# Kernel optimization log

Measured on AMD Instinct MI355X. Metric: run time of the kernel, lower is better.

## Reference

```python
import jax, jax.numpy as jnp
import numpy as np

D_MODEL = 1024
HEADS = 16
HEAD_DIM = D_MODEL // HEADS
SEQ_LEN = 2048
BATCH = 2
LN_EPS = 1e-5


def _layernorm(x, gamma, beta):
    mu = jnp.mean(x, axis=-1, keepdims=True)
    var = jnp.var(x, axis=-1, keepdims=True)
    return (x - mu) * jax.lax.rsqrt(var + LN_EPS) * gamma + beta


def setup_inputs() -> dict:
    key = jax.random.key(0)
    ks = jax.random.split(key, 12)
    d, h = D_MODEL, 4 * D_MODEL
    s = lambda fan_in: 1.0 / np.sqrt(fan_in)
    return {
        "x": jax.random.normal(ks[0], (BATCH, SEQ_LEN, d), dtype=jnp.float32),
        "W_qkv": jax.random.uniform(ks[1], (d, 3 * d), minval=-s(d), maxval=s(d)),
        "b_qkv": jax.random.uniform(ks[2], (3 * d,), minval=-s(d), maxval=s(d)),
        "W1": jax.random.uniform(ks[3], (d, h), minval=-s(d), maxval=s(d)),
        "b1": jax.random.uniform(ks[4], (h,), minval=-s(d), maxval=s(d)),
        "W2": jax.random.uniform(ks[5], (h, d), minval=-s(h), maxval=s(h)),
        "b2": jax.random.uniform(ks[6], (d,), minval=-s(h), maxval=s(h)),
        "ln1_g": jnp.ones((d,), jnp.float32),
        "ln1_b": jnp.zeros((d,), jnp.float32),
        "ln2_g": jnp.ones((d,), jnp.float32),
        "ln2_b": jnp.zeros((d,), jnp.float32),
    }


def reference(x, W_qkv, b_qkv, W1, b1, W2, b2, ln1_g, ln1_b, ln2_g, ln2_b):
    B, T, C = x.shape
    # QKV projection -> [B, T, 3, H, hs] -> q,k,v each [B, H, T, hs]
    qkv = (x @ W_qkv + b_qkv).reshape(B, T, 3, HEADS, HEAD_DIM)
    qkv = jnp.transpose(qkv, (2, 0, 3, 1, 4))
    q, k, v = qkv[0], qkv[1], qkv[2]
    # Naive causal attention with full [B,H,T,T] score matrix (matches source)
    A = jnp.einsum("bhqd,bhkd->bhqk", q, k) / jnp.sqrt(jnp.float32(HEAD_DIM))
    causal = jnp.tril(jnp.ones((T, T), dtype=bool))
    A = jnp.where(causal, A, -jnp.inf)
    A = jax.nn.softmax(A, axis=-1)
    attn = jnp.einsum("bhqk,bhkd->bhqd", A, v)  # [B,H,T,hs]
    attn = jnp.transpose(attn, (0, 2, 1, 3)).reshape(B, T, C)
    # Residual + LN, FFN, residual + LN (dropout=0 / eval)
    h = _layernorm(x + attn, ln1_g, ln1_b)
    ff = jax.nn.relu(h @ W1 + b1) @ W2 + b2
    return _layernorm(h + ff, ln2_g, ln2_b)
```

## Files before the change

### kernel.cpp

```cpp
#include <hip/hip_runtime.h>

#define D_MODEL 1024
#define HEADS   16
#define HEAD_DIM 64
#define SEQ     2048
#define BATCH   2
#define ROWS    (BATCH*SEQ)
#define FFDIM   4096

typedef __attribute__((ext_vector_type(8))) short short8;
typedef __attribute__((ext_vector_type(4))) float f32x4;
typedef __attribute__((ext_vector_type(4))) unsigned short us4;

typedef const __attribute__((address_space(1))) unsigned int* gptr_t;
typedef __attribute__((address_space(3))) unsigned int* lptr_t;

__device__ __forceinline__ unsigned short f2bf(float f){
  unsigned int x = __float_as_uint(f);
  x += 0x7fffu + ((x >> 16) & 1u);
  return (unsigned short)(x >> 16);
}

__device__ __forceinline__ float wave_sum(float x){
  #pragma unroll
  for (int off = 32; off; off >>= 1) x += __shfl_xor(x, off);
  return x;
}

__global__ __launch_bounds__(256) void cast_bf16_kernel(const float* __restrict__ in,
                                                        unsigned short* __restrict__ out, int n4){
  int i = blockIdx.x * 256 + threadIdx.x;
  if (i >= n4) return;
  float4 v = *(const float4*)(in + (size_t)i * 4);
  us4 o;
  o[0] = f2bf(v.x); o[1] = f2bf(v.y); o[2] = f2bf(v.z); o[3] = f2bf(v.w);
  *(us4*)(out + (size_t)i * 4) = o;
}

__global__ __launch_bounds__(256) void transpose_cast_kernel(const float* __restrict__ in,
                                                             unsigned short* __restrict__ out,
                                                             int R, int C){
  __shared__ float tile[32][33];
  const int bc = blockIdx.x * 32, br = blockIdx.y * 32;
  const int tx = threadIdx.x & 31, ty = threadIdx.x >> 5;
  #pragma unroll
  for (int j = 0; j < 4; ++j)
    tile[ty + 8*j][tx] = in[(size_t)(br + ty + 8*j) * C + bc + tx];
  __syncthreads();
  #pragma unroll
  for (int j = 0; j < 4; ++j)
    out[(size_t)(bc + ty + 8*j) * R + br + tx] = f2bf(tile[tx][ty + 8*j]);
}

template<int EPI>
__global__ __launch_bounds__(256) void gemm_kernel(const unsigned short* __restrict__ A,
                                                   const unsigned short* __restrict__ BT,
                                                   const float* __restrict__ bias,
                                                   int M, int N, int K, int kchunk,
                                                   int gx, int gy,
                                                   float* __restrict__ outF,
                                                   unsigned short* __restrict__ qo,
                                                   unsigned short* __restrict__ ko,
                                                   unsigned short* __restrict__ vT){
  __shared__ __align__(16) unsigned short Alds[2][128 * 32];
  __shared__ __align__(16) unsigned short Blds[2][128 * 32];
  const int tid = threadIdx.x;
  const int lane = tid & 63;
  const int wid = tid >> 6;
  const int wr = wid >> 1, wc = wid & 1;
  const int lrow = lane & 15, lgrp = lane >> 4;

  const int nwg = gridDim.x;
  const int cpx = nwg >> 3;
  const int wg = (blockIdx.x & 7) * cpx + (blockIdx.x >> 3);
  const int nx = wg % gx;
  const int rest = wg / gx;
  const int my = rest % gy;
  const int sk = rest / gy;

  const int m0 = my * 128, n0 = nx * 128;
  const int kbase0 = sk * kchunk;
  const int sr = lane >> 2, sc = (lane & 3) * 8;

  f32x4 acc[4][4];
  #pragma unroll
  for (int i = 0; i < 4; ++i)
    #pragma unroll
    for (int j = 0; j < 4; ++j)
      acc[i][j] = f32x4{0.f, 0.f, 0.f, 0.f};

  #pragma unroll
  for (int it = 0; it < 2; ++it){
    const int c = wid * 2 + it;
    const int r = c * 16 + sr;
    __builtin_amdgcn_global_load_lds(
        (gptr_t)(const void*)(A + (size_t)(m0 + r) * K + kbase0 + sc),
        (lptr_t)(void*)(&Alds[0][c * 512]), 16, 0, 0);
    __builtin_amdgcn_global_load_lds(
        (gptr_t)(const void*)(BT + (size_t)(n0 + r) * K + kbase0 + sc),
        (lptr_t)(void*)(&Blds[0][c * 512]), 16, 0, 0);
  }

  const int nk = kchunk >> 5;
  int cur = 0;
  for (int kt = 0; kt < nk; ++kt){
    __syncthreads();
    if (kt + 1 < nk){
      const int kb = kbase0 + (kt + 1) * 32;
      #pragma unroll
      for (int it = 0; it < 2; ++it){
        const int c = wid * 2 + it;
        const int r = c * 16 + sr;
        __builtin_amdgcn_global_load_lds(
            (gptr_t)(const void*)(A + (size_t)(m0 + r) * K + kb + sc),
            (lptr_t)(void*)(&Alds[cur ^ 1][c * 512]), 16, 0, 0);
        __builtin_amdgcn_global_load_lds(
            (gptr_t)(const void*)(BT + (size_t)(n0 + r) * K + kb + sc),
            (lptr_t)(void*)(&Blds[cur ^ 1][c * 512]), 16, 0, 0);
      }
    }
    short8 af[4], bfr[4];
    #pragma unroll
    for (int f = 0; f < 4; ++f){
      af[f]  = *(const short8*)&Alds[cur][(wr * 64 + f * 16 + lrow) * 32 + lgrp * 8];
      bfr[f] = *(const short8*)&Blds[cur][(wc * 64 + f * 16 + lrow) * 32 + lgrp * 8];
    }
    __builtin_amdgcn_s_setprio(1);
    #pragma unroll
    for (int i = 0; i < 4; ++i)
      #pragma unroll
      for (int j = 0; j < 4; ++j)
        acc[i][j] = __builtin_amdgcn_mfma_f32_16x16x32_bf16(af[i], bfr[j], acc[i][j], 0, 0, 0);
    __builtin_amdgcn_s_setprio(0);
    cur ^= 1;
  }

  #pragma unroll
  for (int i = 0; i < 4; ++i){
    const int rg = m0 + wr * 64 + i * 16 + lgrp * 4;
    #pragma unroll
    for (int j = 0; j < 4; ++j){
      const int cg = n0 + wc * 64 + j * 16 + lrow;
      if constexpr (EPI == 0){
        const float bb = bias[cg];
        const int which = cg >> 10, rem = cg & 1023;
        const int hh = rem >> 6, dd = rem & 63;
        const int bb_ = rg >> 11, tt = rg & 2047;
        const size_t bh = (size_t)(bb_ * HEADS + hh);
        if (which == 2){
          us4 pk;
          #pragma unroll
          for (int r = 0; r < 4; ++r) pk[r] = f2bf(acc[i][j][r] + bb);
          *(us4*)(vT + (bh * 64 + dd) * SEQ + tt) = pk;
        } else {
          unsigned short* dst = which ? ko : qo;
          const float sc2 = which ? 1.0f : 0.18033688f;
          #pragma unroll
          for (int r = 0; r < 4; ++r)
            dst[(bh * SEQ + tt + r) * 64 + dd] = f2bf((acc[i][j][r] + bb) * sc2);
        }
      } else {
        float* outP = outF + (size_t)sk * M * N;
        #pragma unroll
        for (int r = 0; r < 4; ++r)
          outP[(size_t)(rg + r) * N + cg] = acc[i][j][r];
      }
    }
  }
}

template<int EPI>
__global__ __launch_bounds__(512, 1) void gemm8p_kernel(const unsigned short* __restrict__ A,
                                                        const unsigned short* __restrict__ BT,
                                                        const float* __restrict__ bias,
                                                        int M, int N, int K, int kchunk,
                                                        int gx, int gy,
                                                        unsigned short* __restrict__ outH){
  __shared__ __align__(16) unsigned short Ab[2][2][256 * 32];
  __shared__ __align__(16) unsigned short Bb[2][2][256 * 32];
  const int tid = threadIdx.x, lane = tid & 63, wid = tid >> 6;
  const int wm = wid >> 2, wn = wid & 3;
  const int lr = lane & 15, g = lane >> 4;

  const int nwg = gridDim.x, cpx = nwg >> 3;
  const int wg = (blockIdx.x & 7) * cpx + (blockIdx.x >> 3);
  const int nx = wg % gx;
  const int rest = wg / gx;
  const int my = rest % gy;
  const int sk = rest / gy;
  const int m0 = my * 256, n0 = nx * 256, kb0 = sk * kchunk;
  const int nk = kchunk >> 6;

  f32x4 acc[8][4];
  #pragma unroll
  for (int i = 0; i < 8; ++i)
    #pragma unroll
    for (int j = 0; j < 4; ++j)
      acc[i][j] = f32x4{0.f, 0.f, 0.f, 0.f};

  auto STAGE = [&](int op, int t, int kh){
    const int d = t & 1;
    unsigned short* base = op ? &Bb[d][kh][0] : &Ab[d][kh][0];
    const unsigned short* src = op ? BT : A;
    const int r0 = op ? n0 : m0;
    #pragma unroll
    for (int j = 0; j < 2; ++j){
      const int L = tid + j * 512;
      const int row = L >> 2, c = L & 3;
      __builtin_amdgcn_global_load_lds(
          (gptr_t)(const void*)(src + (size_t)(r0 + row) * K + kb0 + t * 64 + kh * 32
                                + ((c ^ ((row >> 1) & 3)) << 3)),
          (lptr_t)(void*)(base + L * 8), 16, 0, 0);
    }
  };

  STAGE(0,0,0); STAGE(1,0,0); STAGE(0,0,1); STAGE(1,0,1);
  STAGE(0,1,0); STAGE(1,1,0); STAGE(0,1,1); STAGE(1,1,1);
  asm volatile("s_waitcnt vmcnt(12)" ::: "memory");
  __builtin_amdgcn_s_barrier();

  short8 afr[8], bfr[4];

  #define SYNC_NOV()                                              \
    __builtin_amdgcn_s_barrier();                                 \
    asm volatile("s_waitcnt lgkmcnt(0)" ::: "memory");            \
    __builtin_amdgcn_sched_barrier(0);

  for (int t = 0; t < nk; ++t){
    const int d = t & 1;
    #pragma unroll
    for (int i = 0; i < 8; ++i){
      const int row = wm * 128 + i * 16 + lr;
      afr[i] = *(const short8*)&Ab[d][0][row * 32 + ((g ^ ((row >> 1) & 3)) << 3)];
    }
    #pragma unroll
    for (int j = 0; j < 2; ++j){
      const int row = wn * 64 + j * 16 + lr;
      bfr[j] = *(const short8*)&Bb[d][0][row * 32 + ((g ^ ((row >> 1) & 3)) << 3)];
    }
    if (t >= 1 && t + 1 < nk) STAGE(1, t + 1, 1);
    SYNC_NOV()
    __builtin_amdgcn_s_setprio(1);
    #pragma unroll
    for (int i = 0; i < 8; ++i){
      acc[i][0] = __builtin_amdgcn_mfma_f32_16x16x32_bf16(afr[i], bfr[0], acc[i][0], 0, 0, 0);
      acc[i][1] = __builtin_amdgcn_mfma_f32_16x16x32_bf16(afr[i], bfr[1], acc[i][1], 0, 0, 0);
    }
    __builtin_amdgcn_s_setprio(0);
    __builtin_amdgcn_s_barrier();

    #pragma unroll
    for (int j = 0; j < 2; ++j){
      const int row = wn * 64 + (2 + j) * 16 + lr;
      bfr[2 + j] = *(const short8*)&Bb[d][0][row * 32 + ((g ^ ((row >> 1) & 3)) << 3)];
    }
    if (t + 2 < nk) STAGE(0, t + 2, 0);
    if (t + 2 < nk)      asm volatile("s_waitcnt vmcnt(10)" ::: "memory");
    else if (t + 1 < nk) asm volatile("s_waitcnt vmcnt(8)"  ::: "memory");
    else                 asm volatile("s_waitcnt vmcnt(0)"  ::: "memory");
    SYNC_NOV()
    __builtin_amdgcn_s_setprio(1);
    #pragma unroll
    for (int i = 0; i < 8; ++i){
      acc[i][2] = __builtin_amdgcn_mfma_f32_16x16x32_bf16(afr[i], bfr[2], acc[i][2], 0, 0, 0);
      acc[i][3] = __builtin_amdgcn_mfma_f32_16x16x32_bf16(afr[i], bfr[3], acc[i][3], 0, 0, 0);
    }
    __builtin_amdgcn_s_setprio(0);
    __builtin_amdgcn_s_barrier();

    #pragma unroll
    for (int i = 0; i < 8; ++i){
      const int row = wm * 128 + i * 16 + lr;
      afr[i] = *(const short8*)&Ab[d][1][row * 32 + ((g ^ ((row >> 1) & 3)) << 3)];
    }
    #pragma unroll
    for (int j = 0; j < 2; ++j){
      const int row = wn * 64 + j * 16 + lr;
      bfr[j] = *(const short8*)&Bb[d][1][row * 32 + ((g ^ ((row >> 1) & 3)) << 3)];
    }
    if (t + 2 < nk) STAGE(1, t + 2, 0);
    SYNC_NOV()
    __builtin_amdgcn_s_setprio(1);
    #pragma unroll
    for (int i = 0; i < 8; ++i){
      acc[i][0] = __builtin_amdgcn_mfma_f32_16x16x32_bf16(afr[i], bfr[0], acc[i][0], 0, 0, 0);
      acc[i][1] = __builtin_amdgcn_mfma_f32_16x16x32_bf16(afr[i], bfr[1], acc[i][1], 0, 0, 0);
    }
    __builtin_amdgcn_s_setprio(0);
    __builtin_amdgcn_s_barrier();

    #pragma unroll
    for (int j = 0; j < 2; ++j){
      const int row = wn * 64 + (2 + j) * 16 + lr;
      bfr[2 + j] = *(const short8*)&Bb[d][1][row * 32 + ((g ^ ((row >> 1) & 3)) << 3)];
    }
    if (t + 2 < nk) STAGE(0, t + 2, 1);
    if (t + 2 < nk)      asm volatile("s_waitcnt vmcnt(10)" ::: "memory");
    else if (t + 1 < nk) asm volatile("s_waitcnt vmcnt(4)"  ::: "memory");
    SYNC_NOV()
    __builtin_amdgcn_s_setprio(1);
    #pragma unroll
    for (int i = 0; i < 8; ++i){
      acc[i][2] = __builtin_amdgcn_mfma_f32_16x16x32_bf16(afr[i], bfr[2], acc[i][2], 0, 0, 0);
      acc[i][3] = __builtin_amdgcn_mfma_f32_16x16x32_bf16(afr[i], bfr[3], acc[i][3], 0, 0, 0);
    }
    __builtin_amdgcn_s_setprio(0);
    __builtin_amdgcn_s_barrier();
  }
  #undef SYNC_NOV

  #pragma unroll
  for (int i = 0; i < 8; ++i){
    const int rg = m0 + wm * 128 + i * 16 + g * 4;
    #pragma unroll
    for (int j = 0; j < 4; ++j){
      const int cg = n0 + wn * 64 + j * 16 + lr;
      if constexpr (EPI == 1){
        const float bb = bias[cg];
        #pragma unroll
        for (int r = 0; r < 4; ++r)
          outH[(size_t)(rg + r) * N + cg] = f2bf(fmaxf(acc[i][j][r] + bb, 0.f));
      } else {
        unsigned short* dst = outH + (size_t)sk * M * N;
        #pragma unroll
        for (int r = 0; r < 4; ++r)
          dst[(size_t)(rg + r) * N + cg] = f2bf(acc[i][j][r]);
      }
    }
  }
}

__global__ __launch_bounds__(256) void attn_mfma_kernel(const unsigned short* __restrict__ Qb,
                                                        const unsigned short* __restrict__ Kb,
                                                        const unsigned short* __restrict__ VT,
                                                        float* __restrict__ Op){
  __shared__ __align__(16) char Kl[2][8192];
  __shared__ __align__(16) char Vl[2][8192];
  __shared__ __align__(16) char Pl[4][4096];
  const int tid = threadIdx.x;
  const int w = tid >> 6, lane = tid & 63;
  const int lr = lane & 15, g = lane >> 4;

  const int bx = blockIdx.x, u = bx & 255, half = bx >> 8;
  const int g8 = u >> 5;
  const int qg = half ? g8 : 15 - g8;
  const int bh = u & 31;

  const int q0w = qg * 128 + w * 32;
  const int qA = q0w + lr, qB = qA + 16;

  const char* const KbB = (const char*)(Kb + (size_t)bh * SEQ * 64);
  const char* const VbB = (const char*)(VT + (size_t)bh * 64 * SEQ);
  char* const PbA = Pl[w];
  char* const PbB = Pl[w] + 2048;

  const unsigned short* qra = Qb + ((size_t)bh * SEQ + qA) * 64 + g * 8;
  const short8 qfA0 = *(const short8*)(qra);
  const short8 qfA1 = *(const short8*)(qra + 32);
  const short8 qfB0 = *(const short8*)(qra + 16 * 64);
  const short8 qfB1 = *(const short8*)(qra + 16 * 64 + 32);

  f32x4 oA[4], oB[4];
  #pragma unroll
  for (int dt = 0; dt < 4; ++dt){ oA[dt] = f32x4{0.f,0.f,0.f,0.f}; oB[dt] = f32x4{0.f,0.f,0.f,0.f}; }
  float lA = 0.f, lB = 0.f;
  const int swzl = (lr & 7) << 4;

  const int kbmax = 2 * qg + 1;

  short8 st[4];
  {
    #pragma unroll
    for (int c = 0; c < 2; ++c){
      const int L = c * 4096 + tid * 16;
      st[c] = *(const short8*)(KbB + L);
      const int row = L >> 7, col = L & 127;
      st[2 + c] = *(const short8*)(VbB + (size_t)row * 4096 + col);
    }
  }

  for (int kb = 0; kb <= kbmax; ++kb){
    const int p = kb & 1;
    const int k0 = kb * 64;

    #pragma unroll
    for (int c = 0; c < 2; ++c){
      const int L = c * 4096 + tid * 16;
      const int row = L >> 7, col = L & 127;
      const int dst = row * 128 + (col ^ ((row & 7) << 4));
      *(short8*)(Kl[p] + dst) = st[c];
      *(short8*)(Vl[p] + dst) = st[2 + c];
    }
    __syncthreads();

    if (kb < kbmax){
      #pragma unroll
      for (int c = 0; c < 2; ++c){
        const int L = c * 4096 + tid * 16;
        st[c] = *(const short8*)(KbB + (size_t)(kb + 1) * 8192 + L);
        const int row = L >> 7, col = L & 127;
        st[2 + c] = *(const short8*)(VbB + (size_t)row * 4096 + (size_t)(kb + 1) * 128 + col);
      }
    }

    f32x4 sA[4], sB[4];
    __builtin_amdgcn_s_setprio(1);
    #pragma unroll
    for (int kt = 0; kt < 4; ++kt){
      const int row = kt * 16 + lr;
      const int ro = row * 128, sw = (row & 7) << 4;
      const short8 kf0 = *(const short8*)(Kl[p] + ro + ((g * 16) ^ sw));
      const short8 kf1 = *(const short8*)(Kl[p] + ro + ((64 + g * 16) ^ sw));
      sA[kt] = __builtin_amdgcn_mfma_f32_16x16x32_bf16(kf0, qfA0, f32x4{0.f,0.f,0.f,0.f}, 0, 0, 0);
      sA[kt] = __builtin_amdgcn_mfma_f32_16x16x32_bf16(kf1, qfA1, sA[kt], 0, 0, 0);
      sB[kt] = __builtin_amdgcn_mfma_f32_16x16x32_bf16(kf0, qfB0, f32x4{0.f,0.f,0.f,0.f}, 0, 0, 0);
      sB[kt] = __builtin_amdgcn_mfma_f32_16x16x32_bf16(kf1, qfB1, sB[kt], 0, 0, 0);
    }
    __builtin_amdgcn_s_setprio(0);

    if (kb >= kbmax - 1){
      #pragma unroll
      for (int kt = 0; kt < 4; ++kt)
        #pragma unroll
        for (int r = 0; r < 4; ++r){
          const int key = k0 + kt * 16 + g * 4 + r;
          if (key > qA) sA[kt][r] = -INFINITY;
          if (key > qB) sB[kt][r] = -INFINITY;
        }
    }

    {
      float sum = 0.f;
      #pragma unroll
      for (int kt = 0; kt < 4; ++kt){
        #pragma unroll
        for (int r = 0; r < 4; ++r){
          const float pp = __builtin_amdgcn_exp2f(sA[kt][r]);
          sA[kt][r] = pp; sum += pp;
        }
        unsigned int p01, p23;
        asm("v_cvt_pk_bf16_f32 %0, %1, %2" : "=v"(p01) : "v"(sA[kt][0]), "v"(sA[kt][1]));
        asm("v_cvt_pk_bf16_f32 %0, %1, %2" : "=v"(p23) : "v"(sA[kt][2]), "v"(sA[kt][3]));
        uint2 pk; pk.x = p01; pk.y = p23;
        *(uint2*)(PbA + lr * 128 + ((kt * 32 + g * 8) ^ swzl)) = pk;
      }
      sum += __shfl_xor(sum, 16);
      sum += __shfl_xor(sum, 32);
      lA += sum;
    }
    {
      float sum = 0.f;
      #pragma unroll
      for (int kt = 0; kt < 4; ++kt){
        #pragma unroll
        for (int r = 0; r < 4; ++r){
          const float pp = __builtin_amdgcn_exp2f(sB[kt][r]);
          sB[kt][r] = pp; sum += pp;
        }
        unsigned int p01, p23;
        asm("v_cvt_pk_bf16_f32 %0, %1, %2" : "=v"(p01) : "v"(sB[kt][0]), "v"(sB[kt][1]));
        asm("v_cvt_pk_bf16_f32 %0, %1, %2" : "=v"(p23) : "v"(sB[kt][2]), "v"(sB[kt][3]));
        uint2 pk; pk.x = p01; pk.y = p23;
        *(uint2*)(PbB + lr * 128 + ((kt * 32 + g * 8) ^ swzl)) = pk;
      }
      sum += __shfl_xor(sum, 16);
      sum += __shfl_xor(sum, 32);
      lB += sum;
    }

    const short8 paA0 = *(const short8*)(PbA + lr * 128 + ((g * 16) ^ swzl));
    const short8 paA1 = *(const short8*)(PbA + lr * 128 + ((64 + g * 16) ^ swzl));
    const short8 paB0 = *(const short8*)(PbB + lr * 128 + ((g * 16) ^ swzl));
    const short8 paB1 = *(const short8*)(PbB + lr * 128 + ((64 + g * 16) ^ swzl));
    __builtin_amdgcn_s_setprio(1);
    #pragma unroll
    for (int dt = 0; dt < 4; ++dt){
      const int row = dt * 16 + lr;
      const int ro = row * 128, sw = (row & 7) << 4;
      const short8 vf0 = *(const short8*)(Vl[p] + ro + ((g * 16) ^ sw));
      const short8 vf1 = *(const short8*)(Vl[p] + ro + ((64 + g * 16) ^ sw));
      oA[dt] = __builtin_amdgcn_mfma_f32_16x16x32_bf16(paA0, vf0, oA[dt], 0, 0, 0);
      oA[dt] = __builtin_amdgcn_mfma_f32_16x16x32_bf16(paA1, vf1, oA[dt], 0, 0, 0);
      oB[dt] = __builtin_amdgcn_mfma_f32_16x16x32_bf16(paB0, vf0, oB[dt], 0, 0, 0);
      oB[dt] = __builtin_amdgcn_mfma_f32_16x16x32_bf16(paB1, vf1, oB[dt], 0, 0, 0);
    }
    __builtin_amdgcn_s_setprio(0);
  }

  const int b = bh >> 4, hh = bh & 15;
  {
    float lv[4];
    #pragma unroll
    for (int r = 0; r < 4; ++r) lv[r] = __shfl(lA, g * 4 + r);
    #pragma unroll
    for (int dt = 0; dt < 4; ++dt)
      #pragma unroll
      for (int r = 0; r < 4; ++r)
        Op[((size_t)(b * SEQ) + q0w + g * 4 + r) * D_MODEL + hh * 64 + dt * 16 + lr] = oA[dt][r] / lv[r];
  }
  {
    float lv[4];
    #pragma unroll
    for (int r = 0; r < 4; ++r) lv[r] = __shfl(lB, g * 4 + r);
    #pragma unroll
    for (int dt = 0; dt < 4; ++dt)
      #pragma unroll
      for (int r = 0; r < 4; ++r)
        Op[((size_t)(b * SEQ) + q0w + 16 + g * 4 + r) * D_MODEL + hh * 64 + dt * 16 + lr] = oB[dt][r] / lv[r];
  }
}

__global__ __launch_bounds__(256) void ln_kernel(const float* __restrict__ A,
                                                 const float* __restrict__ B1,
                                                 const unsigned short* __restrict__ P4,
                                                 size_t pstride,
                                                 const float* __restrict__ bias,
                                                 const float* __restrict__ g,
                                                 const float* __restrict__ be,
                                                 float* __restrict__ outF,
                                                 unsigned short* __restrict__ outH){
  const int row = blockIdx.x, tid = threadIdx.x;
  const size_t base = (size_t)row * D_MODEL + tid * 4;
  float4 va = *(const float4*)(A + base);
  float v0 = va.x, v1 = va.y, v2 = va.z, v3 = va.w;
  if (B1){
    float4 vb = *(const float4*)(B1 + base);
    v0 += vb.x; v1 += vb.y; v2 += vb.z; v3 += vb.w;
  }
  if (P4){
    #pragma unroll
    for (int p = 0; p < 4; ++p){
      us4 u = *(const us4*)(P4 + p * pstride + base);
      v0 += __uint_as_float((unsigned int)u[0] << 16);
      v1 += __uint_as_float((unsigned int)u[1] << 16);
      v2 += __uint_as_float((unsigned int)u[2] << 16);
      v3 += __uint_as_float((unsigned int)u[3] << 16);
    }
  }
  if (bias){
    float4 vd = *(const float4*)(bias + tid * 4);
    v0 += vd.x; v1 += vd.y; v2 += vd.z; v3 += vd.w;
  }
  float s  = v0 + v1 + v2 + v3;
  float ss = v0*v0 + v1*v1 + v2*v2 + v3*v3;
  s = wave_sum(s); ss = wave_sum(ss);
  __shared__ float red[8];
  const int w = tid >> 6, lane = tid & 63;
  if (!lane){ red[w] = s; red[4 + w] = ss; }
  __syncthreads();
  s  = red[0] + red[1] + red[2] + red[3];
  ss = red[4] + red[5] + red[6] + red[7];
  const float mu  = s * (1.0f / D_MODEL);
  const float var = ss * (1.0f / D_MODEL) - mu * mu;
  const float rstd = rsqrtf(var + 1e-5f);
  float4 gg = *(const float4*)(g  + tid * 4);
  float4 bb = *(const float4*)(be + tid * 4);
  const float r0 = (v0 - mu) * rstd * gg.x + bb.x;
  const float r1 = (v1 - mu) * rstd * gg.y + bb.y;
  const float r2 = (v2 - mu) * rstd * gg.z + bb.z;
  const float r3 = (v3 - mu) * rstd * gg.w + bb.w;
  float4 of; of.x = r0; of.y = r1; of.z = r2; of.w = r3;
  *(float4*)(outF + base) = of;
  if (outH){
    us4 oh; oh[0] = f2bf(r0); oh[1] = f2bf(r1); oh[2] = f2bf(r2); oh[3] = f2bf(r3);
    *(us4*)(outH + base) = oh;
  }
}

__global__ __launch_bounds__(256) void ln2f_kernel(const float* __restrict__ A,
                                                   const float* __restrict__ B1,
                                                   const float* __restrict__ bias,
                                                   const float* __restrict__ g,
                                                   const float* __restrict__ be,
                                                   float* __restrict__ outF){
  const int row = blockIdx.x, tid = threadIdx.x;
  const size_t base = (size_t)row * D_MODEL + tid * 4;
  float4 va = *(const float4*)(A + base);
  float4 vb = *(const float4*)(B1 + base);
  float4 vd = *(const float4*)(bias + tid * 4);
  float v0 = va.x + vb.x + vd.x, v1 = va.y + vb.y + vd.y;
  float v2 = va.z + vb.z + vd.z, v3 = va.w + vb.w + vd.w;
  float s  = v0 + v1 + v2 + v3;
  float ss = v0*v0 + v1*v1 + v2*v2 + v3*v3;
  s = wave_sum(s); ss = wave_sum(ss);
  __shared__ float red[8];
  const int w = tid >> 6, lane = tid & 63;
  if (!lane){ red[w] = s; red[4 + w] = ss; }
  __syncthreads();
  s  = red[0] + red[1] + red[2] + red[3];
  ss = red[4] + red[5] + red[6] + red[7];
  const float mu  = s * (1.0f / D_MODEL);
  const float var = ss * (1.0f / D_MODEL) - mu * mu;
  const float rstd = rsqrtf(var + 1e-5f);
  float4 gg = *(const float4*)(g  + tid * 4);
  float4 bb = *(const float4*)(be + tid * 4);
  float4 of;
  of.x = (v0 - mu) * rstd * gg.x + bb.x;
  of.y = (v1 - mu) * rstd * gg.y + bb.y;
  of.z = (v2 - mu) * rstd * gg.z + bb.z;
  of.w = (v3 - mu) * rstd * gg.w + bb.w;
  *(float4*)(outF + base) = of;
}

extern "C" void kernel_launch(void* const* d_in, const int* in_sizes, int n_in,
                              void* d_out, int out_size, void* d_ws, size_t ws_size,
                              hipStream_t stream){
  (void)in_sizes; (void)n_in; (void)out_size;
  const float* x     = (const float*)d_in[0];
  const float* W_qkv = (const float*)d_in[1];
  const float* b_qkv = (const float*)d_in[2];
  const float* W1    = (const float*)d_in[3];
  const float* b1    = (const float*)d_in[4];
  const float* W2    = (const float*)d_in[5];
  const float* b2    = (const float*)d_in[6];
  const float* ln1g  = (const float*)d_in[7];
  const float* ln1b  = (const float*)d_in[8];
  const float* ln2g  = (const float*)d_in[9];
  const float* ln2b  = (const float*)d_in[10];

  char* ws = (char*)d_ws;
  const size_t MB = 1024ull * 1024ull;
  unsigned short* WqkvT = (unsigned short*)(ws + 0 * MB);
  unsigned short* W1T   = (unsigned short*)(ws + 6 * MB);
  unsigned short* W2T   = (unsigned short*)(ws + 14 * MB);
  unsigned short* xbf   = (unsigned short*)(ws + 22 * MB);
  unsigned short* qB    = (unsigned short*)(ws + 30 * MB);
  unsigned short* kB    = (unsigned short*)(ws + 39 * MB);
  unsigned short* vT    = (unsigned short*)(ws + 48 * MB);
  float* attn = (float*)(ws + 57 * MB);
  float* hF           = (float*)(ws + 30 * MB);
  unsigned short* hB  = (unsigned short*)(ws + 46 * MB);
  unsigned short* ff1 = (unsigned short*)(ws + 54 * MB);
  unsigned short* pbf = (unsigned short*)(ws + 86 * MB);
  float* p0           = (float*)(ws + 86 * MB);

  const int use8p = (ws_size >= 118 * MB);

  cast_bf16_kernel<<<4096, 256, 0, stream>>>(x, xbf, ROWS * D_MODEL / 4);
  transpose_cast_kernel<<<dim3(96, 32), 256, 0, stream>>>(W_qkv, WqkvT, 1024, 3072);
  transpose_cast_kernel<<<dim3(128, 32), 256, 0, stream>>>(W1, W1T, 1024, 4096);
  transpose_cast_kernel<<<dim3(32, 128), 256, 0, stream>>>(W2, W2T, 4096, 1024);

  gemm_kernel<0><<<768, 256, 0, stream>>>(
      xbf, WqkvT, b_qkv, ROWS, 3072, 1024, 1024, 24, 32, nullptr, qB, kB, vT);

  attn_mfma_kernel<<<512, 256, 0, stream>>>(qB, kB, vT, attn);

  ln_kernel<<<ROWS, 256, 0, stream>>>(x, attn, nullptr, 0, nullptr, ln1g, ln1b, hF, hB);

  gemm8p_kernel<1><<<256, 512, 0, stream>>>(
      hB, W1T, b1, ROWS, FFDIM, 1024, 1024, 16, 16, ff1);

  if (use8p){
    gemm8p_kernel<4><<<256, 512, 0, stream>>>(
        ff1, W2T, nullptr, ROWS, 1024, FFDIM, 1024, 4, 16, pbf);
    ln_kernel<<<ROWS, 256, 0, stream>>>(hF, nullptr, pbf, (size_t)ROWS * 1024, b2,
                                        ln2g, ln2b, (float*)d_out, nullptr);
  } else {
    gemm_kernel<3><<<256, 256, 0, stream>>>(
        ff1, W2T, nullptr, ROWS, 1024, FFDIM, FFDIM, 8, 32, p0, nullptr, nullptr, nullptr);
    ln2f_kernel<<<ROWS, 256, 0, stream>>>(hF, p0, b2, ln2g, ln2b, (float*)d_out);
  }
}
```

Baseline: 200.5 us.

## Restructure FFN GEMM main loop into two-phase double-buffered register pipeline

Replaces the four-phase per-iteration schedule of the 256x256 FFN GEMM with a two-phase one. Each phase issues 32 MFMAs on one K-half while LDS reads for the next half go into a second register set. Global-to-LDS prefetch is now one tile ahead per half instead of two, which cuts barriers per K step from eight to two. The cost is extra VGPRs for the duplicated fragment registers and a shallower global prefetch depth, which may expose memory latency.

New measurement: 215.1 us. 7.2% more time.

```diff
diff --git a/kernel.cpp b/kernel.cpp
--- a/kernel.cpp
+++ b/kernel.cpp
@@ -170,7 +170,7 @@
 }
 
 template<int EPI>
-__global__ __launch_bounds__(512, 1) void gemm8p_kernel(const unsigned short* __restrict__ A,
+__global__ __launch_bounds__(512, 1) void gemm2h_kernel(const unsigned short* __restrict__ A,
                                                         const unsigned short* __restrict__ BT,
                                                         const float* __restrict__ bias,
                                                         int M, int N, int K, int kchunk,
@@ -199,8 +199,8 @@
       acc[i][j] = f32x4{0.f, 0.f, 0.f, 0.f};
 
   auto STAGE = [&](int op, int t, int kh){
-    const int d = t & 1;
-    unsigned short* base = op ? &Bb[d][kh][0] : &Ab[d][kh][0];
+    const int d_ = t & 1;
+    unsigned short* base = op ? &Bb[d_][kh][0] : &Ab[d_][kh][0];
     const unsigned short* src = op ? BT : A;
     const int r0 = op ? n0 : m0;
     #pragma unroll
@@ -214,100 +214,65 @@
     }
   };
 
+  short8 afA[8], bfA[4], afB[8], bfB[4];
+
+  #define READS(da, db, d_, kh_)                                                          \
+    _Pragma("unroll")                                                                     \
+    for (int i = 0; i < 8; ++i){                                                          \
+      const int row = wm * 128 + i * 16 + lr;                                             \
+      da[i] = *(const short8*)&Ab[d_][kh_][row * 32 + ((g ^ ((row >> 1) & 3)) << 3)];     \
+    }                                                                                     \
+    _Pragma("unroll")                                                                     \
+    for (int j = 0; j < 4; ++j){                                                          \
+      const int row = wn * 64 + j * 16 + lr;                                              \
+      db[j] = *(const short8*)&Bb[d_][kh_][row * 32 + ((g ^ ((row >> 1) & 3)) << 3)];     \
+    }
+
+  #define MFMA32(sa, sb)                                                                  \
+    _Pragma("unroll")                                                                     \
+    for (int i = 0; i < 8; ++i)                                                           \
+      _Pragma("unroll")                                                                   \
+      for (int j = 0; j < 4; ++j)                                                         \
+        acc[i][j] = __builtin_amdgcn_mfma_f32_16x16x32_bf16(sa[i], sb[j], acc[i][j], 0, 0, 0);
+
   STAGE(0,0,0); STAGE(1,0,0); STAGE(0,0,1); STAGE(1,0,1);
-  STAGE(0,1,0); STAGE(1,1,0); STAGE(0,1,1); STAGE(1,1,1);
-  asm volatile("s_waitcnt vmcnt(12)" ::: "memory");
+  if (nk > 1){ STAGE(0,1,0); STAGE(1,1,0); }
+  if (nk > 1) asm volatile("s_waitcnt vmcnt(8)" ::: "memory");
+  else        asm volatile("s_waitcnt vmcnt(4)" ::: "memory");
   __builtin_amdgcn_s_barrier();
-
-  short8 afr[8], bfr[4];
-
-  #define SYNC_NOV()                                              \
-    __builtin_amdgcn_s_barrier();                                 \
-    asm volatile("s_waitcnt lgkmcnt(0)" ::: "memory");            \
+  READS(afA, bfA, 0, 0)
+
+  for (int t = 0; t < nk; ++t){
+    const int d = t & 1, dn = d ^ 1;
+
+    if (t + 1 < nk) asm volatile("s_waitcnt vmcnt(4)" ::: "memory");
+    else            asm volatile("s_waitcnt vmcnt(0)" ::: "memory");
+    __builtin_amdgcn_s_barrier();
+    if (t + 1 < nk){ STAGE(0, t + 1, 1); STAGE(1, t + 1, 1); }
+    READS(afB, bfB, d, 1)
+    asm volatile("s_waitcnt lgkmcnt(12)" ::: "memory");
     __builtin_amdgcn_sched_barrier(0);
-
-  for (int t = 0; t < nk; ++t){
-    const int d = t & 1;
-    #pragma unroll
-    for (int i = 0; i < 8; ++i){
-      const int row = wm * 128 + i * 16 + lr;
-      afr[i] = *(const short8*)&Ab[d][0][row * 32 + ((g ^ ((row >> 1) & 3)) << 3)];
-    }
-    #pragma unroll
-    for (int j = 0; j < 2; ++j){
-      const int row = wn * 64 + j * 16 + lr;
-      bfr[j] = *(const short8*)&Bb[d][0][row * 32 + ((g ^ ((row >> 1) & 3)) << 3)];
-    }
-    if (t >= 1 && t + 1 < nk) STAGE(1, t + 1, 1);
-    SYNC_NOV()
     __builtin_amdgcn_s_setprio(1);
-    #pragma unroll
-    for (int i = 0; i < 8; ++i){
-      acc[i][0] = __builtin_amdgcn_mfma_f32_16x16x32_bf16(afr[i], bfr[0], acc[i][0], 0, 0, 0);
-      acc[i][1] = __builtin_amdgcn_mfma_f32_16x16x32_bf16(afr[i], bfr[1], acc[i][1], 0, 0, 0);
-    }
+    MFMA32(afA, bfA)
     __builtin_amdgcn_s_setprio(0);
+
+    if (t + 1 < nk) asm volatile("s_waitcnt vmcnt(4)" ::: "memory");
+    else            asm volatile("s_waitcnt vmcnt(0)" ::: "memory");
     __builtin_amdgcn_s_barrier();
-
-    #pragma unroll
-    for (int j = 0; j < 2; ++j){
-      const int row = wn * 64 + (2 + j) * 16 + lr;
-      bfr[2 + j] = *(const short8*)&Bb[d][0][row * 32 + ((g ^ ((row >> 1) & 3)) << 3)];
-    }
-    if (t + 2 < nk) STAGE(0, t + 2, 0);
-    if (t + 2 < nk)      asm volatile("s_waitcnt vmcnt(10)" ::: "memory");
-    else if (t + 1 < nk) asm volatile("s_waitcnt vmcnt(8)"  ::: "memory");
-    else                 asm volatile("s_waitcnt vmcnt(0)"  ::: "memory");
-    SYNC_NOV()
+    if (t + 2 < nk){ STAGE(0, t + 2, 0); STAGE(1, t + 2, 0); }
+    if (t + 1 < nk){
+      READS(afA, bfA, dn, 0)
+      asm volatile("s_waitcnt lgkmcnt(12)" ::: "memory");
+    } else {
+      asm volatile("s_waitcnt lgkmcnt(0)" ::: "memory");
+    }
+    __builtin_amdgcn_sched_barrier(0);
     __builtin_amdgcn_s_setprio(1);
-    #pragma unroll
-    for (int i = 0; i < 8; ++i){
-      acc[i][2] = __builtin_amdgcn_mfma_f32_16x16x32_bf16(afr[i], bfr[2], acc[i][2], 0, 0, 0);
-      acc[i][3] = __builtin_amdgcn_mfma_f32_16x16x32_bf16(afr[i], bfr[3], acc[i][3], 0, 0, 0);
-    }
+    MFMA32(afB, bfB)
     __builtin_amdgcn_s_setprio(0);
-    __builtin_amdgcn_s_barrier();
-
-    #pragma unroll
-    for (int i = 0; i < 8; ++i){
-      const int row = wm * 128 + i * 16 + lr;
-      afr[i] = *(const short8*)&Ab[d][1][row * 32 + ((g ^ ((row >> 1) & 3)) << 3)];
-    }
-    #pragma unroll
-    for (int j = 0; j < 2; ++j){
-      const int row = wn * 64 + j * 16 + lr;
-      bfr[j] = *(const short8*)&Bb[d][1][row * 32 + ((g ^ ((row >> 1) & 3)) << 3)];
-    }
-    if (t + 2 < nk) STAGE(1, t + 2, 0);
-    SYNC_NOV()
-    __builtin_amdgcn_s_setprio(1);
-    #pragma unroll
-    for (int i = 0; i < 8; ++i){
-      acc[i][0] = __builtin_amdgcn_mfma_f32_16x16x32_bf16(afr[i], bfr[0], acc[i][0], 0, 0, 0);
-      acc[i][1] = __builtin_amdgcn_mfma_f32_16x16x32_bf16(afr[i], bfr[1], acc[i][1], 0, 0, 0);
-    }
-    __builtin_amdgcn_s_setprio(0);
-    __builtin_amdgcn_s_barrier();
-
-    #pragma unroll
-    for (int j = 0; j < 2; ++j){
-      const int row = wn * 64 + (2 + j) * 16 + lr;
-      bfr[2 + j] = *(const short8*)&Bb[d][1][row * 32 + ((g ^ ((row >> 1) & 3)) << 3)];
-    }
-    if (t + 2 < nk) STAGE(0, t + 2, 1);
-    if (t + 2 < nk)      asm volatile("s_waitcnt vmcnt(10)" ::: "memory");
-    else if (t + 1 < nk) asm volatile("s_waitcnt vmcnt(4)"  ::: "memory");
-    SYNC_NOV()
-    __builtin_amdgcn_s_setprio(1);
-    #pragma unroll
-    for (int i = 0; i < 8; ++i){
-      acc[i][2] = __builtin_amdgcn_mfma_f32_16x16x32_bf16(afr[i], bfr[2], acc[i][2], 0, 0, 0);
-      acc[i][3] = __builtin_amdgcn_mfma_f32_16x16x32_bf16(afr[i], bfr[3], acc[i][3], 0, 0, 0);
-    }
-    __builtin_amdgcn_s_setprio(0);
-    __builtin_amdgcn_s_barrier();
-  }
-  #undef SYNC_NOV
+  }
+  #undef READS
+  #undef MFMA32
 
   #pragma unroll
   for (int i = 0; i < 8; ++i){
@@ -634,7 +599,7 @@
   unsigned short* pbf = (unsigned short*)(ws + 86 * MB);
   float* p0           = (float*)(ws + 86 * MB);
 
-  const int use8p = (ws_size >= 118 * MB);
+  const int use2h = (ws_size >= 118 * MB);
 
   cast_bf16_kernel<<<4096, 256, 0, stream>>>(x, xbf, ROWS * D_MODEL / 4);
   transpose_cast_kernel<<<dim3(96, 32), 256, 0, stream>>>(W_qkv, WqkvT, 1024, 3072);
@@ -648,11 +613,11 @@
 
   ln_kernel<<<ROWS, 256, 0, stream>>>(x, attn, nullptr, 0, nullptr, ln1g, ln1b, hF, hB);
 
-  gemm8p_kernel<1><<<256, 512, 0, stream>>>(
+  gemm2h_kernel<1><<<256, 512, 0, stream>>>(
       hB, W1T, b1, ROWS, FFDIM, 1024, 1024, 16, 16, ff1);
 
-  if (use8p){
-    gemm8p_kernel<4><<<256, 512, 0, stream>>>(
+  if (use2h){
+    gemm2h_kernel<4><<<256, 512, 0, stream>>>(
         ff1, W2T, nullptr, ROWS, 1024, FFDIM, 1024, 4, 16, pbf);
     ln_kernel<<<ROWS, 256, 0, stream>>>(hF, nullptr, pbf, (size_t)ROWS * 1024, b2,
                                         ln2g, ln2b, (float*)d_out, nullptr);
```
